# Kernel optimization log

Hardware: AMD Instinct MI355X
Metric: run time of the kernel (lower is better)

## Reference

```python
import jax, jax.numpy as jnp
import numpy as np

D_MODEL = 512
NUM_HEADS = 8
DEPTH = D_MODEL // NUM_HEADS
BATCH = 16
SEQ = 1024


def setup_inputs() -> dict:
    key = jax.random.key(0)
    kq, kk, kv, k1, k2, k3, k4 = jax.random.split(key, 7)
    scale = 1.0 / np.sqrt(D_MODEL)
    return {
        "v": jax.random.normal(kv, (BATCH, SEQ, D_MODEL), jnp.float32),
        "k": jax.random.normal(kk, (BATCH, SEQ, D_MODEL), jnp.float32),
        "q": jax.random.normal(kq, (BATCH, SEQ, D_MODEL), jnp.float32),
        "mask": jnp.ones((BATCH, SEQ), jnp.float32),
        # Conv1D(kernel_size=1, use_bias=False) == per-token Linear: x @ W, W [d_in, d_out]
        "Wq": jax.random.normal(k1, (D_MODEL, D_MODEL), jnp.float32) * scale,
        "Wk": jax.random.normal(k2, (D_MODEL, D_MODEL), jnp.float32) * scale,
        "Wv": jax.random.normal(k3, (D_MODEL, D_MODEL), jnp.float32) * scale,
        "Wo": jax.random.normal(k4, (D_MODEL, D_MODEL), jnp.float32) * scale,
    }


def _split_heads(x, batch):
    # [b, s, d_model] -> [b, h, s, depth]
    return x.reshape(batch, -1, NUM_HEADS, DEPTH).transpose(0, 2, 1, 3)


def reference(v, k, q, mask, Wq, Wk, Wv, Wo):
    batch = q.shape[0]
    qh = _split_heads(q @ Wq, batch)  # [b,h,sq,dh]
    kh = _split_heads(k @ Wk, batch)  # [b,h,sk,dh]
    vh = _split_heads(v @ Wv, batch)  # [b,h,sk,dh]

    dk = jnp.asarray(DEPTH, qh.dtype)
    logits = jnp.einsum("bhqd,bhkd->bhqk", qh, kh) / jnp.sqrt(dk)
    # additive padding mask, broadcast [b,1,1,sk]
    logits = logits + (1.0 - mask[:, None, None, :]) * (-1e9)
    attention_weights = jax.nn.softmax(logits, axis=-1)  # [b,h,sq,sk]

    ctx = jnp.einsum("bhqk,bhkd->bhqd", attention_weights, vh)
    ctx = ctx.transpose(0, 2, 1, 3).reshape(batch, -1, D_MODEL)
    output = ctx @ Wo
    return output, attention_weights
```

## Files before the change

### kernel.cpp

```cpp
#include <hip/hip_runtime.h>


typedef _Float16 f16;
typedef _Float16 f16x8 __attribute__((ext_vector_type(8)));
typedef float f32x4 __attribute__((ext_vector_type(4)));

#define DEVINL __device__ __forceinline__

static constexpr int BATCH = 16, SEQ = 1024, DM = 512, NH = 8, DH = 64;

DEVINL void async16(void* lds, const void* g) {
  __builtin_amdgcn_global_load_lds(
      (const __attribute__((address_space(1))) unsigned int*)g,
      (__attribute__((address_space(3))) unsigned int*)lds, 16, 0, 0);
}

__global__ __launch_bounds__(256) void prep_wt_k(
    const float* __restrict__ Wq, const float* __restrict__ Wk,
    const float* __restrict__ Wv, const float* __restrict__ Wo,
    f16* __restrict__ WT) {
  __shared__ float t[32][33];
  const int w = blockIdx.z;
  const float* src = (w == 0) ? Wq : (w == 1) ? Wk : (w == 2) ? Wv : Wo;
  const int k0 = blockIdx.y * 32, n0 = blockIdx.x * 32;
  const int r0 = threadIdx.x >> 5, c = threadIdx.x & 31;
#pragma unroll
  for (int i = 0; i < 4; ++i)
    t[i * 8 + r0][c] = src[(size_t)(k0 + i * 8 + r0) * DM + n0 + c];
  __syncthreads();
  f16* dst = WT + (size_t)w * DM * DM;
#pragma unroll
  for (int i = 0; i < 4; ++i)
    dst[(size_t)(n0 + i * 8 + r0) * DM + k0 + c] = (f16)t[c][i * 8 + r0];
}

template <int MODE>
DEVINL void gemm_body(const float* __restrict__ A32, const f16* __restrict__ A16,
                      const f16* __restrict__ WTn, f16* __restrict__ O16,
                      float* __restrict__ O32, int m0, int n0) {
  __shared__ __align__(16) f16 As[2][128 * 32];
  __shared__ __align__(16) f16 Bs[2][128 * 32];
  const int tid = threadIdx.x;
  const int lane = tid & 63, wave = tid >> 6;
  const int wr = wave >> 1, wc = wave & 1;
  const int lrow = lane & 15, lkg = lane >> 4;
  f32x4 acc[4][4] = {};

  f32x4 ar[4];

  auto stageB = [&](int kt, int buf) {
#pragma unroll
    for (int it = 0; it < 2; ++it) {
      const int o = (it * 256 + tid) * 16;
      const int n = o >> 6, kb = o & 63;
      async16((char*)&Bs[buf][0] + (it * 256 + wave * 64) * 16,
              (const char*)WTn + ((size_t)(n0 + n) * DM + kt * 32) * 2 + kb);
    }
  };
  auto stageA_async = [&](int kt, int buf) {
#pragma unroll
    for (int it = 0; it < 2; ++it) {
      const int o = (it * 256 + tid) * 16;
      const int row = o >> 6, kb = o & 63;
      async16((char*)&As[buf][0] + (it * 256 + wave * 64) * 16,
              (const char*)A16 + ((size_t)(m0 + row) * DM + kt * 32) * 2 + kb);
    }
  };
  auto loadA = [&](int kt) {
    const int row = tid >> 1, kh = (tid & 1) * 16;
    const float* s = A32 + (size_t)(m0 + row) * DM + kt * 32 + kh;
    ar[0] = *(const f32x4*)(s);
    ar[1] = *(const f32x4*)(s + 4);
    ar[2] = *(const f32x4*)(s + 8);
    ar[3] = *(const f32x4*)(s + 12);
  };
  auto writeA = [&](int buf) {
    const int row = tid >> 1, kh = (tid & 1) * 16;
#pragma unroll
    for (int half = 0; half < 2; ++half) {
      f16x8 t;
      t[0] = (f16)ar[half * 2][0]; t[1] = (f16)ar[half * 2][1];
      t[2] = (f16)ar[half * 2][2]; t[3] = (f16)ar[half * 2][3];
      t[4] = (f16)ar[half * 2 + 1][0]; t[5] = (f16)ar[half * 2 + 1][1];
      t[6] = (f16)ar[half * 2 + 1][2]; t[7] = (f16)ar[half * 2 + 1][3];
      *(f16x8*)&As[buf][row * 32 + kh + half * 8] = t;
    }
  };

  stageB(0, 0);
  if (MODE == 0) {
    loadA(0);
    writeA(0);
  } else {
    stageA_async(0, 0);
  }
  __syncthreads();

  for (int kt = 0; kt < DM / 32; ++kt) {
    const int cur = kt & 1;
    if (kt < DM / 32 - 1) {
      stageB(kt + 1, cur ^ 1);
      if (MODE == 0) loadA(kt + 1);
      else stageA_async(kt + 1, cur ^ 1);
    }
    f16x8 af[4], bf[4];
#pragma unroll
    for (int i = 0; i < 4; ++i)
      af[i] = *(const f16x8*)&As[cur][(wr * 64 + i * 16 + lrow) * 32 + lkg * 8];
#pragma unroll
    for (int j = 0; j < 4; ++j)
      bf[j] = *(const f16x8*)&Bs[cur][(wc * 64 + j * 16 + lrow) * 32 + lkg * 8];
#pragma unroll
    for (int i = 0; i < 4; ++i)
#pragma unroll
      for (int j = 0; j < 4; ++j)
        acc[i][j] = __builtin_amdgcn_mfma_f32_16x16x32_f16(af[i], bf[j], acc[i][j], 0, 0, 0);
    if (MODE == 0 && kt < DM / 32 - 1) writeA(cur ^ 1);
    __syncthreads();
  }

#pragma unroll
  for (int i = 0; i < 4; ++i) {
#pragma unroll
    for (int j = 0; j < 4; ++j) {
#pragma unroll
      for (int r = 0; r < 4; ++r) {
        const int m = m0 + wr * 64 + i * 16 + lkg * 4 + r;
        const int g = n0 + wc * 64 + j * 16 + lrow;
        if (MODE == 0) {
          const int b = m >> 10, s = m & 1023, hh = g >> 6, d = g & 63;
          O16[(((size_t)b * NH + hh) * SEQ + s) * DH + d] = (f16)acc[i][j][r];
        } else {
          O32[(size_t)m * DM + g] = acc[i][j][r];
        }
      }
    }
  }
}

__global__ __launch_bounds__(256, 2) void proj_k(
    const float* __restrict__ q, const float* __restrict__ k, const float* __restrict__ v,
    const f16* __restrict__ WT, f16* __restrict__ Qh, f16* __restrict__ Kh,
    f16* __restrict__ Vh) {
  const int bid = blockIdx.x;
  const int wid = (bid & 7) * 192 + (bid >> 3);
  const int n_blk = wid & 3, m_blk = (wid >> 2) & 127, z = wid >> 9;
  const float* A = (z == 0) ? q : (z == 1) ? k : v;
  const f16* W = WT + (size_t)z * DM * DM;
  f16* O = (z == 0) ? Qh : (z == 1) ? Kh : Vh;
  gemm_body<0>(A, nullptr, W, O, nullptr, m_blk * 128, n_blk * 128);
}

__global__ __launch_bounds__(256, 2) void outp_k(const f16* __restrict__ ctx,
                                                 const f16* __restrict__ WoT,
                                                 float* __restrict__ out0) {
  const int bid = blockIdx.x;
  const int wid = (bid & 7) * 64 + (bid >> 3);
  const int n_blk = wid & 3, m_blk = wid >> 2;
  gemm_body<1>(nullptr, ctx, WoT, nullptr, out0, m_blk * 128, n_blk * 128);
}

__global__ __launch_bounds__(256, 2) void attn_k(
    const f16* __restrict__ Qh, const f16* __restrict__ Kh, const f16* __restrict__ Vh,
    const float* __restrict__ mask, float* __restrict__ attnW, f16* __restrict__ ctx) {
  __shared__ __align__(16) f16 Ks[2][64 * 64];
  __shared__ __align__(16) f16 Vt[2][64 * 64];
  __shared__ __align__(16) f16 Ps[4][16 * 64];
  const int tid = threadIdx.x;
  const int lane = tid & 63, wave = tid >> 6;
  const int lrow = lane & 15, lkg = lane >> 4;
  const int bid = blockIdx.x;
  const int wid = (bid & 7) * 256 + (bid >> 3);
  const int qt = wid & 15, h = (wid >> 4) & 7, b = wid >> 7;
  const size_t bh = (size_t)b * NH + h;
  const f16* Kbase = Kh + bh * SEQ * DH;
  const f16* Vbase = Vh + bh * SEQ * DH;
  const int q0 = qt * 64 + wave * 16;

  auto stageK = [&](int kt, int buf) {
    const char* KtileB = (const char*)(Kbase + (size_t)kt * 64 * DH);
#pragma unroll
    for (int it = 0; it < 2; ++it) {
      const int o = (it * 256 + tid) * 16;
      const int key = o >> 7, slot = (o >> 4) & 7;
      async16((char*)&Ks[buf][0] + (it * 256 + wave * 64) * 16,
              KtileB + key * 128 + ((slot ^ (key & 7)) << 4));
    }
  };

  f16x8 aQ0, aQ1;
  {
    const f16* qp = Qh + (bh * SEQ + q0 + lrow) * DH + lkg * 8;
    aQ0 = *(const f16x8*)qp;
    aQ1 = *(const f16x8*)(qp + 32);
  }

  float sums[4] = {0.f, 0.f, 0.f, 0.f};

  stageK(0, 0);
  __syncthreads();
  for (int kt = 0; kt < 16; ++kt) {
    const int cur = kt & 1;
    if (kt < 15) stageK(kt + 1, cur ^ 1);
    f32x4 lg[4] = {};
#pragma unroll
    for (int j = 0; j < 4; ++j) {
      const int key = j * 16 + lrow;
      f16x8 b0 = *(const f16x8*)((const char*)&Ks[cur][0] + key * 128 + ((lkg ^ (key & 7)) << 4));
      f16x8 b1 = *(const f16x8*)((const char*)&Ks[cur][0] + key * 128 + (((4 + lkg) ^ (key & 7)) << 4));
      lg[j] = __builtin_amdgcn_mfma_f32_16x16x32_f16(aQ0, b0, lg[j], 0, 0, 0);
      lg[j] = __builtin_amdgcn_mfma_f32_16x16x32_f16(aQ1, b1, lg[j], 0, 0, 0);
    }
#pragma unroll
    for (int j = 0; j < 4; ++j) {
      const int key = kt * 64 + j * 16 + lrow;
      const float bias = (1.0f - mask[b * SEQ + key]) * (-1e9f);
#pragma unroll
      for (int r = 0; r < 4; ++r) sums[r] += __expf(lg[j][r] * 0.125f + bias);
    }
    __syncthreads();
  }

#pragma unroll
  for (int r = 0; r < 4; ++r) {
    float s = sums[r];
    s += __shfl_xor(s, 1);
    s += __shfl_xor(s, 2);
    s += __shfl_xor(s, 4);
    s += __shfl_xor(s, 8);
    sums[r] = 1.0f / s;
  }

  f32x4 ctxacc[4] = {};
  float* awBase = attnW + (bh * SEQ + q0) * SEQ;

  const int vkey = tid >> 2, vd0 = (tid & 3) * 16;
  f16x8 vr0, vr1;
  auto loadV = [&](int kt) {
    const f16* vp = Vbase + ((size_t)kt * 64 + vkey) * DH + vd0;
    vr0 = *(const f16x8*)vp;
    vr1 = *(const f16x8*)(vp + 8);
  };
  auto writeVt = [&](int buf) {
#pragma unroll
    for (int jj = 0; jj < 8; ++jj) {
      const int d = vd0 + jj;
      *(f16*)((char*)&Vt[buf][0] + d * 128 + (((vkey >> 3) ^ (d & 7)) << 4) + (vkey & 7) * 2) = vr0[jj];
    }
#pragma unroll
    for (int jj = 0; jj < 8; ++jj) {
      const int d = vd0 + 8 + jj;
      *(f16*)((char*)&Vt[buf][0] + d * 128 + (((vkey >> 3) ^ (d & 7)) << 4) + (vkey & 7) * 2) = vr1[jj];
    }
  };

  stageK(0, 0);
  loadV(0);
  writeVt(0);
  __syncthreads();
  for (int kt = 0; kt < 16; ++kt) {
    const int cur = kt & 1;
    if (kt < 15) {
      stageK(kt + 1, cur ^ 1);
      loadV(kt + 1);
    }
    f32x4 lg[4] = {};
#pragma unroll
    for (int j = 0; j < 4; ++j) {
      const int key = j * 16 + lrow;
      f16x8 b0 = *(const f16x8*)((const char*)&Ks[cur][0] + key * 128 + ((lkg ^ (key & 7)) << 4));
      f16x8 b1 = *(const f16x8*)((const char*)&Ks[cur][0] + key * 128 + (((4 + lkg) ^ (key & 7)) << 4));
      lg[j] = __builtin_amdgcn_mfma_f32_16x16x32_f16(aQ0, b0, lg[j], 0, 0, 0);
      lg[j] = __builtin_amdgcn_mfma_f32_16x16x32_f16(aQ1, b1, lg[j], 0, 0, 0);
    }
    float* aw = awBase + kt * 64;
#pragma unroll
    for (int j = 0; j < 4; ++j) {
      const int keyc = j * 16 + lrow;
      const float bias = (1.0f - mask[b * SEQ + kt * 64 + keyc]) * (-1e9f);
#pragma unroll
      for (int r = 0; r < 4; ++r) {
        const int row = lkg * 4 + r;
        const float w = __expf(lg[j][r] * 0.125f + bias) * sums[r];
        aw[(size_t)row * SEQ + keyc] = w;
        *(f16*)((char*)&Ps[wave][0] + row * 128 + (((keyc >> 3) ^ (row & 7)) << 4) +
                (keyc & 7) * 2) = (f16)w;
      }
    }
#pragma unroll
    for (int kk = 0; kk < 2; ++kk) {
      const int kidx = kk * 32 + lkg * 8;
      f16x8 aP = *(const f16x8*)((const char*)&Ps[wave][0] + lrow * 128 +
                                 (((kidx >> 3) ^ (lrow & 7)) << 4));
#pragma unroll
      for (int j2 = 0; j2 < 4; ++j2) {
        const int d = j2 * 16 + lrow;
        f16x8 bV = *(const f16x8*)((const char*)&Vt[cur][0] + d * 128 + (((kidx >> 3) ^ (d & 7)) << 4));
        ctxacc[j2] = __builtin_amdgcn_mfma_f32_16x16x32_f16(aP, bV, ctxacc[j2], 0, 0, 0);
      }
    }
    if (kt < 15) writeVt(cur ^ 1);
    __syncthreads();
  }

#pragma unroll
  for (int j2 = 0; j2 < 4; ++j2)
#pragma unroll
    for (int r = 0; r < 4; ++r) {
      const int s = q0 + lkg * 4 + r;
      const int d = j2 * 16 + lrow;
      ctx[(((size_t)b * SEQ + s) * NH + h) * DH + d] = (f16)ctxacc[j2][r];
    }
}

extern "C" void kernel_launch(void* const* d_in, const int* in_sizes, int n_in,
                              void* d_out, int out_size, void* d_ws, size_t ws_size,
                              hipStream_t stream) {
  const float* v = (const float*)d_in[0];
  const float* k = (const float*)d_in[1];
  const float* q = (const float*)d_in[2];
  const float* mask = (const float*)d_in[3];
  const float* Wq = (const float*)d_in[4];
  const float* Wk = (const float*)d_in[5];
  const float* Wv = (const float*)d_in[6];
  const float* Wo = (const float*)d_in[7];

  float* out0 = (float*)d_out;
  float* attnW = out0 + (size_t)BATCH * SEQ * DM;

  char* ws = (char*)d_ws;
  f16* WT = (f16*)ws;
  f16* Qh = (f16*)(ws + (size_t)4 * DM * DM * 2);
  f16* Kh = Qh + (size_t)BATCH * NH * SEQ * DH;
  f16* Vh = Kh + (size_t)BATCH * NH * SEQ * DH;
  f16* ctx = Vh + (size_t)BATCH * NH * SEQ * DH;

  prep_wt_k<<<dim3(16, 16, 4), 256, 0, stream>>>(Wq, Wk, Wv, Wo, WT);
  proj_k<<<dim3(1536), 256, 0, stream>>>(q, k, v, WT, Qh, Kh, Vh);
  attn_k<<<dim3(2048), 256, 0, stream>>>(Qh, Kh, Vh, mask, attnW, ctx);
  outp_k<<<dim3(512), 256, 0, stream>>>(ctx, WT + (size_t)3 * DM * DM, out0);
}
```

Measured before the change: 319.7 us.

## Vectorize attention-weight stores via LDS, use nontemporal stores, raise attn occupancy

Attention weights are now written as coalesced 16-byte nontemporal stores, read back from the f16 P tile in LDS, instead of scattered scalar fp32 stores. The GEMM fp32 A loads are remapped so adjacent threads read adjacent 16-byte chunks, and GEMM epilogue stores become nontemporal. attn_k launch bounds are raised to 4 blocks per CU. The stored attention weights now pass through f16 rounding, which lowers precision of that output, and the higher occupancy target may cause register spills.

```diff
diff --git a/kernel.cpp b/kernel.cpp
--- a/kernel.cpp
+++ b/kernel.cpp
@@ -3,6 +3,7 @@
 
 typedef _Float16 f16;
 typedef _Float16 f16x8 __attribute__((ext_vector_type(8)));
+typedef _Float16 f16x4 __attribute__((ext_vector_type(4)));
 typedef float f32x4 __attribute__((ext_vector_type(4)));
 
 #define DEVINL __device__ __forceinline__
@@ -67,23 +68,22 @@
     }
   };
   auto loadA = [&](int kt) {
-    const int row = tid >> 1, kh = (tid & 1) * 16;
-    const float* s = A32 + (size_t)(m0 + row) * DM + kt * 32 + kh;
-    ar[0] = *(const f32x4*)(s);
-    ar[1] = *(const f32x4*)(s + 4);
-    ar[2] = *(const f32x4*)(s + 8);
-    ar[3] = *(const f32x4*)(s + 12);
+#pragma unroll
+    for (int c = 0; c < 4; ++c) {
+      const int idx = c * 256 + tid;
+      const int row = idx >> 3, sub = idx & 7;
+      ar[c] = *(const f32x4*)(A32 + (size_t)(m0 + row) * DM + kt * 32 + sub * 4);
+    }
   };
   auto writeA = [&](int buf) {
-    const int row = tid >> 1, kh = (tid & 1) * 16;
-#pragma unroll
-    for (int half = 0; half < 2; ++half) {
-      f16x8 t;
-      t[0] = (f16)ar[half * 2][0]; t[1] = (f16)ar[half * 2][1];
-      t[2] = (f16)ar[half * 2][2]; t[3] = (f16)ar[half * 2][3];
-      t[4] = (f16)ar[half * 2 + 1][0]; t[5] = (f16)ar[half * 2 + 1][1];
-      t[6] = (f16)ar[half * 2 + 1][2]; t[7] = (f16)ar[half * 2 + 1][3];
-      *(f16x8*)&As[buf][row * 32 + kh + half * 8] = t;
+#pragma unroll
+    for (int c = 0; c < 4; ++c) {
+      const int idx = c * 256 + tid;
+      const int row = idx >> 3, sub = idx & 7;
+      f16x4 t;
+      t[0] = (f16)ar[c][0]; t[1] = (f16)ar[c][1];
+      t[2] = (f16)ar[c][2]; t[3] = (f16)ar[c][3];
+      *(f16x4*)&As[buf][row * 32 + sub * 4] = t;
     }
   };
 
@@ -129,9 +129,10 @@
         const int g = n0 + wc * 64 + j * 16 + lrow;
         if (MODE == 0) {
           const int b = m >> 10, s = m & 1023, hh = g >> 6, d = g & 63;
-          O16[(((size_t)b * NH + hh) * SEQ + s) * DH + d] = (f16)acc[i][j][r];
+          __builtin_nontemporal_store(
+              (f16)acc[i][j][r], &O16[(((size_t)b * NH + hh) * SEQ + s) * DH + d]);
         } else {
-          O32[(size_t)m * DM + g] = acc[i][j][r];
+          __builtin_nontemporal_store(acc[i][j][r], &O32[(size_t)m * DM + g]);
         }
       }
     }
@@ -160,7 +161,7 @@
   gemm_body<1>(nullptr, ctx, WoT, nullptr, out0, m_blk * 128, n_blk * 128);
 }
 
-__global__ __launch_bounds__(256, 2) void attn_k(
+__global__ __launch_bounds__(256, 4) void attn_k(
     const f16* __restrict__ Qh, const f16* __restrict__ Kh, const f16* __restrict__ Vh,
     const float* __restrict__ mask, float* __restrict__ attnW, f16* __restrict__ ctx) {
   __shared__ __align__(16) f16 Ks[2][64 * 64];
@@ -273,7 +274,6 @@
       lg[j] = __builtin_amdgcn_mfma_f32_16x16x32_f16(aQ0, b0, lg[j], 0, 0, 0);
       lg[j] = __builtin_amdgcn_mfma_f32_16x16x32_f16(aQ1, b1, lg[j], 0, 0, 0);
     }
-    float* aw = awBase + kt * 64;
 #pragma unroll
     for (int j = 0; j < 4; ++j) {
       const int keyc = j * 16 + lrow;
@@ -282,10 +282,25 @@
       for (int r = 0; r < 4; ++r) {
         const int row = lkg * 4 + r;
         const float w = __expf(lg[j][r] * 0.125f + bias) * sums[r];
-        aw[(size_t)row * SEQ + keyc] = w;
         *(f16*)((char*)&Ps[wave][0] + row * 128 + (((keyc >> 3) ^ (row & 7)) << 4) +
                 (keyc & 7) * 2) = (f16)w;
       }
+    }
+    {
+      const int row = lane >> 2, slice = lane & 3;
+      const char* prow = (const char*)&Ps[wave][0] + row * 128;
+      f16x8 p0 = *(const f16x8*)(prow + (((slice * 2) ^ (row & 7)) << 4));
+      f16x8 p1 = *(const f16x8*)(prow + (((slice * 2 + 1) ^ (row & 7)) << 4));
+      float* dst = awBase + (size_t)row * SEQ + kt * 64 + slice * 16;
+      f32x4 o0, o1, o2, o3;
+      o0[0] = (float)p0[0]; o0[1] = (float)p0[1]; o0[2] = (float)p0[2]; o0[3] = (float)p0[3];
+      o1[0] = (float)p0[4]; o1[1] = (float)p0[5]; o1[2] = (float)p0[6]; o1[3] = (float)p0[7];
+      o2[0] = (float)p1[0]; o2[1] = (float)p1[1]; o2[2] = (float)p1[2]; o2[3] = (float)p1[3];
+      o3[0] = (float)p1[4]; o3[1] = (float)p1[5]; o3[2] = (float)p1[6]; o3[3] = (float)p1[7];
+      __builtin_nontemporal_store(o0, (f32x4*)dst);
+      __builtin_nontemporal_store(o1, (f32x4*)(dst + 4));
+      __builtin_nontemporal_store(o2, (f32x4*)(dst + 8));
+      __builtin_nontemporal_store(o3, (f32x4*)(dst + 12));
     }
 #pragma unroll
     for (int kk = 0; kk < 2; ++kk) {
```

Result: slower. 687.8 us (+115.2%).
